# Optimization experiments

Measured on AMD Instinct MI355X. Metric: run time of the kernel, lower is better.

## Reference

```python
import jax, jax.numpy as jnp
import numpy as np

B, L, DIM, DQK = 4, 8192, 512, 512
THRESH = 0.5
TARGET_N = 6.0
RATIO_W = 0.03
LR_DIFF = 0.75
EPS = 1e-8


def setup_inputs() -> dict:
    key = jax.random.key(0)
    k1, k2, k3 = jax.random.split(key, 3)
    tokens = jax.random.normal(k1, (B, L, DIM), dtype=jnp.float32)
    # Linear(dim, 2*dqk, bias=False) weight, torch layout [out, in]
    Wqk = jax.random.normal(k2, (2 * DQK, DIM), dtype=jnp.float32) / np.sqrt(DIM).astype(np.float32)
    start_key = jax.random.normal(k3, (DQK,), dtype=jnp.float32) * 0.01  # heads=1
    return {"tokens": tokens, "Wqk": Wqk, "start_key": start_key}


def _straight_through(t, value):
    return t + jax.lax.stop_gradient(value - t)


def _frac_gradient(t, frac):
    # forward = t, backward grad scaled by frac
    return _straight_through(t * frac, t)


def _cosine_sim(a, b):
    dot = jnp.sum(a * b, axis=-1)
    na = jnp.maximum(jnp.sqrt(jnp.sum(a * a, axis=-1)), EPS)
    nb = jnp.maximum(jnp.sqrt(jnp.sum(b * b, axis=-1)), EPS)
    return dot / (na * nb)


def _assoc_scan(gates, x):
    # h_t = gates_t * h_{t-1} + x_t along axis 1 (inclusive first-order scan)
    def comb(l, r):
        al, bl = l
        ar, br = r
        return al * ar, br + ar * bl
    _, h = jax.lax.associative_scan(comb, (gates[..., None], x), axis=1)
    return h


def reference(tokens, Wqk, start_key):
    Bn, Ln, D = tokens.shape
    qk = jnp.einsum('bnd,ed->bne', tokens, Wqk)          # [B, L, 2*DQK]
    queries, keys = qk[..., :DQK], qk[..., DQK:]
    # key for position i is key_{i-1}, with learned start key at position 0
    keys_shift = jnp.concatenate(
        [jnp.broadcast_to(start_key, (Bn, 1, DQK)), keys[:, :-1]], axis=1)
    cos = _cosine_sim(queries, keys_shift)               # [B, L]
    probs = (1.0 - cos) * 0.5
    boundary = (probs > THRESH).at[:, 0].set(True)       # [B, L] bool
    num_chunks = boundary.sum(axis=-1)                   # [B]

    # stable compaction: boundary positions first, in order
    order = jnp.argsort(jnp.logical_not(boundary).astype(jnp.int32), axis=1)  # [B, L]
    ar = jnp.arange(Ln)
    chunk_mask = ar[None, :] < num_chunks[:, None]       # valid chunk slots
    pos = jnp.where(chunk_mask, order, Ln)               # boundary positions, sentinel L
    next_pos = jnp.concatenate([pos[:, 1:], jnp.full((Bn, 1), Ln, dtype=pos.dtype)], axis=1)
    chunk_lens = jnp.where(chunk_mask, next_pos - pos, 0)  # [B, L] int

    gathered = jnp.take_along_axis(tokens, order[..., None], axis=1)  # [B, L, D]
    boundary_probs = jnp.where(chunk_mask, jnp.take_along_axis(probs, order, axis=1), 0.0)
    gates = 1.0 - boundary_probs                         # padded slots -> 1 (matches torch, never read)
    downsampled = gathered * boundary_probs[..., None]   # padded slots -> 0

    confidence = jnp.where(boundary, probs, 1.0 - probs)
    scale = _straight_through(confidence, 1.0)           # forward value 1.0

    # aux ratio loss (with straight-through soft boundary fraction)
    Nt = TARGET_N
    F_hard = boundary.astype(probs.dtype)
    F_soft = jax.nn.sigmoid(probs - THRESH)
    F = _straight_through(F_soft, F_hard)
    Gm = probs.mean(axis=-1)
    Fm = F.mean(axis=-1)
    aux = (Nt / (Nt - 1.0)) * ((Nt - 1.0) * Fm * Gm + (1.0 - Fm) * (1.0 - Gm))
    weighted_aux_loss = aux.mean() * RATIO_W

    downsampled_out = _frac_gradient(downsampled, 1.0 / LR_DIFF)

    # ---- upsample path (the returned closure in the torch module) ----
    scanned = _assoc_scan(gates, downsampled_out)        # smooth across chunks
    rank = jnp.cumsum(boundary.astype(jnp.int32), axis=1) - 1  # chunk id of each token
    upsampled = jnp.take_along_axis(scanned, rank[..., None], axis=1)  # [B, L, D]
    upsampled = upsampled * scale[..., None]
    upsampled = _frac_gradient(upsampled, LR_DIFF)

    return downsampled_out, upsampled, weighted_aux_loss
```

## Files before the change

kernel.cpp:

```cpp
#include <hip/hip_runtime.h>
#include <cstdint>
#include <cstddef>

#define L 8192
#define BATCH 4
#define DQK 512
#define M_TOT (BATCH*L)
#define NSEG 128
#define SEGC 64
#define EPSC 1e-8f

typedef __attribute__((ext_vector_type(8))) short bf16x8;
typedef __attribute__((ext_vector_type(4))) float f32x4;
typedef __attribute__((ext_vector_type(8))) unsigned short u16x8;

__device__ __forceinline__ unsigned short bf16_rne(float x) {
  union { float f; unsigned u; } v; v.f = x;
  unsigned r = v.u + 0x7fffu + ((v.u >> 16) & 1u);
  return (unsigned short)(r >> 16);
}
__device__ __forceinline__ float bf16_tof(unsigned short b) {
  union { unsigned u; float f; } v; v.u = ((unsigned)b) << 16;
  return v.f;
}
__device__ __forceinline__ void gload_lds16(const void* g, void* l) {
  __builtin_amdgcn_global_load_lds(
      (const __attribute__((address_space(1))) unsigned int*)g,
      (__attribute__((address_space(3))) unsigned int*)l, 16, 0, 0);
}

__global__ __launch_bounds__(256) void k_split(const float* __restrict__ tokens,
                                               const float* __restrict__ Wqk,
                                               unsigned short* __restrict__ A1,
                                               unsigned short* __restrict__ A2,
                                               unsigned short* __restrict__ A3,
                                               unsigned short* __restrict__ W1,
                                               unsigned short* __restrict__ W2,
                                               unsigned short* __restrict__ W3) {
  const float* src; unsigned short *d1, *d2, *d3; size_t e0;
  if (blockIdx.x < 8192) {
    src = tokens; d1 = A1; d2 = A2; d3 = A3;
    e0 = ((size_t)blockIdx.x * 256 + threadIdx.x) * 8;
  } else {
    src = Wqk; d1 = W1; d2 = W2; d3 = W3;
    e0 = ((size_t)(blockIdx.x - 8192) * 256 + threadIdx.x) * 8;
  }
  float v[8];
  *(float4*)&v[0] = *(const float4*)(src + e0);
  *(float4*)&v[4] = *(const float4*)(src + e0 + 4);
  unsigned short o1[8], o2[8], o3[8];
  #pragma unroll
  for (int j = 0; j < 8; ++j) {
    float x = v[j];
    unsigned short b1 = bf16_rne(x);
    float r1 = x - bf16_tof(b1);
    unsigned short b2 = bf16_rne(r1);
    float r2 = r1 - bf16_tof(b2);
    unsigned short b3 = bf16_rne(r2);
    o1[j] = b1; o2[j] = b2; o3[j] = b3;
  }
  *(u16x8*)(d1 + e0) = *(u16x8*)o1;
  *(u16x8*)(d2 + e0) = *(u16x8*)o2;
  *(u16x8*)(d3 + e0) = *(u16x8*)o3;
}

__global__ __launch_bounds__(256, 3) void k_gemm_bf16(
    const unsigned short* __restrict__ A1, const unsigned short* __restrict__ A2,
    const unsigned short* __restrict__ A3,
    const unsigned short* __restrict__ W1, const unsigned short* __restrict__ W2,
    const unsigned short* __restrict__ W3,
    float* __restrict__ C) {
  __shared__ unsigned short lds[6 * 512 * 8];
  const int g = (blockIdx.x & 7) * 256 + (blockIdx.x >> 3);
  const int bx = g & 7;
  const int by = g >> 3;
  const int t = threadIdx.x;
  const int lane = t & 63;
  const int w = t >> 6;
  const int wr = w >> 1, wc = w & 1;

  f32x4 acc[4][4];
  #pragma unroll
  for (int i = 0; i < 4; ++i)
    #pragma unroll
    for (int j = 0; j < 4; ++j) acc[i][j] = (f32x4){0.f, 0.f, 0.f, 0.f};

  const unsigned short* srcA[3] = {A1, A2, A3};
  const unsigned short* srcW[3] = {W1, W2, W3};
  const int arow = by * 128;
  const int wrow = bx * 128;
  const int kg = lane >> 4;
  const int fr = lane & 15;

  for (int ks = 0; ks < 16; ++ks) {
    __syncthreads();
    const int kofs = ks * 32;
    #pragma unroll
    for (int s = 0; s < 3; ++s) {
      #pragma unroll
      for (int it = 0; it < 2; ++it) {
        const int p = it * 256 + t;
        const int row = p & 127, pg = p >> 7;
        gload_lds16(srcA[s] + (size_t)(arow + row) * 512 + kofs + pg * 8,
                    &lds[(s * 512 + p) * 8]);
        gload_lds16(srcW[s] + (size_t)(wrow + row) * 512 + kofs + pg * 8,
                    &lds[((3 + s) * 512 + p) * 8]);
      }
    }
    __syncthreads();

    bf16x8 bfr[4][3];
    #pragma unroll
    for (int nf = 0; nf < 4; ++nf) {
      const int row = wc * 64 + nf * 16 + fr;
      #pragma unroll
      for (int s = 0; s < 3; ++s)
        bfr[nf][s] = *(const bf16x8*)&lds[(((3 + s) * 512) + kg * 128 + row) * 8];
    }
    #pragma unroll
    for (int mf = 0; mf < 4; ++mf) {
      const int row = wr * 64 + mf * 16 + fr;
      bf16x8 a1 = *(const bf16x8*)&lds[((0 * 512) + kg * 128 + row) * 8];
      bf16x8 a2 = *(const bf16x8*)&lds[((1 * 512) + kg * 128 + row) * 8];
      bf16x8 a3 = *(const bf16x8*)&lds[((2 * 512) + kg * 128 + row) * 8];
      #pragma unroll
      for (int nf = 0; nf < 4; ++nf) {
        f32x4 c = acc[mf][nf];
        c = __builtin_amdgcn_mfma_f32_16x16x32_bf16(a1, bfr[nf][0], c, 0, 0, 0);
        c = __builtin_amdgcn_mfma_f32_16x16x32_bf16(a1, bfr[nf][1], c, 0, 0, 0);
        c = __builtin_amdgcn_mfma_f32_16x16x32_bf16(a2, bfr[nf][0], c, 0, 0, 0);
        c = __builtin_amdgcn_mfma_f32_16x16x32_bf16(a2, bfr[nf][1], c, 0, 0, 0);
        c = __builtin_amdgcn_mfma_f32_16x16x32_bf16(a1, bfr[nf][2], c, 0, 0, 0);
        c = __builtin_amdgcn_mfma_f32_16x16x32_bf16(a3, bfr[nf][0], c, 0, 0, 0);
        acc[mf][nf] = c;
      }
    }
  }
  const int fq = lane >> 4;
  #pragma unroll
  for (int mf = 0; mf < 4; ++mf) {
    #pragma unroll
    for (int nf = 0; nf < 4; ++nf) {
      const int col = bx * 128 + wc * 64 + nf * 16 + fr;
      #pragma unroll
      for (int r = 0; r < 4; ++r) {
        const int rrow = by * 128 + wr * 64 + mf * 16 + fq * 4 + r;
        C[(size_t)rrow * 1024 + col] = acc[mf][nf][r];
      }
    }
  }
}

__global__ __launch_bounds__(256) void k_gemm(const float* __restrict__ A,
                                              const float* __restrict__ W,
                                              float* __restrict__ C) {
  __shared__ float As[8][128];
  __shared__ float Bs[8][128];
  const int bx = blockIdx.x & 7;
  const int by = blockIdx.x >> 3;
  const int t  = threadIdx.x;
  const int tx = t & 15, ty = t >> 4;
  const int lr = t >> 1;
  const int lc = (t & 1) * 4;
  const float* Ag = A + (size_t)(by*128 + lr)*512 + lc;
  const float* Wg = W + (size_t)(bx*128 + lr)*512 + lc;
  float acc[8][8];
  #pragma unroll
  for (int i=0;i<8;i++)
    #pragma unroll
    for (int j=0;j<8;j++) acc[i][j]=0.f;

  for (int k0 = 0; k0 < 512; k0 += 8) {
    float4 av = *(const float4*)(Ag + k0);
    float4 bv = *(const float4*)(Wg + k0);
    __syncthreads();
    As[lc+0][lr]=av.x; As[lc+1][lr]=av.y; As[lc+2][lr]=av.z; As[lc+3][lr]=av.w;
    Bs[lc+0][lr]=bv.x; Bs[lc+1][lr]=bv.y; Bs[lc+2][lr]=bv.z; Bs[lc+3][lr]=bv.w;
    __syncthreads();
    #pragma unroll
    for (int kk=0;kk<8;kk++) {
      float af[8], bf[8];
      *(float4*)&af[0] = *(const float4*)&As[kk][ty*8];
      *(float4*)&af[4] = *(const float4*)&As[kk][ty*8+4];
      *(float4*)&bf[0] = *(const float4*)&Bs[kk][tx*8];
      *(float4*)&bf[4] = *(const float4*)&Bs[kk][tx*8+4];
      #pragma unroll
      for (int i=0;i<8;i++)
        #pragma unroll
        for (int j=0;j<8;j++)
          acc[i][j] = fmaf(af[i], bf[j], acc[i][j]);
    }
  }
  const int crow = by*128 + ty*8;
  const int ccol = bx*128 + tx*8;
  #pragma unroll
  for (int i=0;i<8;i++) {
    float* cp = C + (size_t)(crow+i)*1024 + ccol;
    *(float4*)cp     = make_float4(acc[i][0],acc[i][1],acc[i][2],acc[i][3]);
    *(float4*)(cp+4) = make_float4(acc[i][4],acc[i][5],acc[i][6],acc[i][7]);
  }
}

__global__ __launch_bounds__(256) void k_cos(const float* __restrict__ qk,
                                             const float* __restrict__ start_key,
                                             float* __restrict__ probs) {
  const int wid = threadIdx.x >> 6;
  const int lane = threadIdx.x & 63;
  const int p = blockIdx.x*4 + wid;
  const int n = p & (L-1);
  const float* q  = qk + (size_t)p*1024;
  const float* ks = (n==0) ? start_key : (qk + (size_t)(p-1)*1024 + 512);
  float dot=0.f, nq=0.f, nk=0.f;
  const int e0 = lane*8;
  #pragma unroll
  for (int j=0;j<8;j+=4) {
    float4 qv = *(const float4*)(q+e0+j);
    float4 kv = *(const float4*)(ks+e0+j);
    dot = fmaf(qv.x,kv.x,dot); dot = fmaf(qv.y,kv.y,dot);
    dot = fmaf(qv.z,kv.z,dot); dot = fmaf(qv.w,kv.w,dot);
    nq  = fmaf(qv.x,qv.x,nq);  nq  = fmaf(qv.y,qv.y,nq);
    nq  = fmaf(qv.z,qv.z,nq);  nq  = fmaf(qv.w,qv.w,nq);
    nk  = fmaf(kv.x,kv.x,nk);  nk  = fmaf(kv.y,kv.y,nk);
    nk  = fmaf(kv.z,kv.z,nk);  nk  = fmaf(kv.w,kv.w,nk);
  }
  #pragma unroll
  for (int m=32;m>=1;m>>=1) {
    dot += __shfl_xor(dot,m);
    nq  += __shfl_xor(nq,m);
    nk  += __shfl_xor(nk,m);
  }
  if (lane==0) {
    float na = fmaxf(sqrtf(nq), EPSC);
    float nb = fmaxf(sqrtf(nk), EPSC);
    float c  = dot/(na*nb);
    probs[p] = 0.5f*(1.f - c);
  }
}

__global__ __launch_bounds__(1024) void k_scan_bd(const float* __restrict__ probs,
                                                  int* __restrict__ bpos,
                                                  int* __restrict__ num_chunks,
                                                  float* __restrict__ auxvals) {
  const int b = blockIdx.x;
  const float* pb = probs + b*L;
  const int t = threadIdx.x;
  float pv[8]; int bd[8];
  const int base = t*8;
  float psum=0.f; int cnt=0;
  #pragma unroll
  for (int j=0;j<8;j++) {
    pv[j] = pb[base+j];
    bd[j] = (base+j == 0) || (pv[j] > 0.5f);
    cnt += bd[j];
    psum += pv[j];
  }
  const int lane = t & 63, w = t >> 6;
  int x = cnt;
  #pragma unroll
  for (int off=1; off<64; off<<=1) {
    int y = __shfl_up(x, off);
    if (lane >= off) x += y;
  }
  float ps = psum;
  #pragma unroll
  for (int m=32;m>=1;m>>=1) ps += __shfl_xor(ps, m);
  __shared__ int wsum[16]; __shared__ int wpre[17]; __shared__ float fsum[16];
  if (lane == 63) wsum[w] = x;
  if (lane == 0)  fsum[w] = ps;
  __syncthreads();
  if (t == 0) {
    int run = 0; float tot = 0.f;
    for (int i=0;i<16;i++) { wpre[i] = run; run += wsum[i]; tot += fsum[i]; }
    wpre[16] = run;
    num_chunks[b] = run;
    float Gm = tot / (float)L;
    float Fm = (float)run / (float)L;
    auxvals[b] = 1.2f * (5.f*Fm*Gm + (1.f-Fm)*(1.f-Gm));
  }
  __syncthreads();
  int rank = wpre[w] + (x - cnt);
  #pragma unroll
  for (int j=0;j<8;j++) {
    if (bd[j]) { bpos[b*L + rank] = base + j; rank++; }
  }
}

__global__ __launch_bounds__(512) void k_scan_local(const float* __restrict__ tokens,
                                                    const float* __restrict__ probs,
                                                    const int* __restrict__ bpos,
                                                    const int* __restrict__ num_chunks,
                                                    float* __restrict__ hend,
                                                    float* __restrict__ Pseg,
                                                    float* __restrict__ down) {
  const int b = blockIdx.x / NSEG;
  const int s = blockIdx.x - b * NSEG;
  const int c = threadIdx.x;
  const int nc = num_chunks[b];
  const int i0 = s*SEGC;
  const int seg = b*NSEG + s;
  const int z0 = (i0 > nc) ? i0 : nc;
  for (int i = z0; i < i0 + SEGC; ++i)
    down[((size_t)(b*L + i))*512 + c] = 0.f;
  if (i0 >= nc) {
    hend[(size_t)seg*512 + c] = 0.f;
    if (c==0) Pseg[seg] = 1.f;
    return;
  }
  const int iend = (i0+SEGC < nc) ? i0+SEGC : nc;
  const int cntc = iend - i0;
  __shared__ float p_s[SEGC];
  __shared__ int n_s[SEGC];
  if (c < cntc) {
    int n = bpos[b*L + i0 + c];
    n_s[c] = n;
    p_s[c] = probs[b*L + n];
  }
  __syncthreads();
  float h = 0.f, gp = 1.f;
  for (int i = i0; i < iend; ++i) {
    const int ii = i - i0;
    const float p = p_s[ii];
    const float g = 1.f - p;
    const float x = tokens[((size_t)(b*L + n_s[ii]))*512 + c] * p;
    h = fmaf(g, h, x);
    gp *= g;
    down[((size_t)(b*L + i))*512 + c] = x;
  }
  hend[(size_t)seg*512 + c] = h;
  if (c==0) Pseg[seg] = gp;
}

__global__ __launch_bounds__(512) void k_seg_scan(const float* __restrict__ hend,
                                                  const float* __restrict__ Pseg,
                                                  float* __restrict__ carry_in) {
  const int b   = blockIdx.x >> 7;
  const int gch = blockIdx.x & 127;
  const int sg  = threadIdx.x & 127;
  const int cl  = threadIdx.x >> 7;
  const int ch  = gch*4 + cl;
  const int seg = b*NSEG + sg;
  float h = hend[(size_t)seg*512 + ch];
  float P = Pseg[seg];
  __shared__ float sh[512], sP[512];
  const int idx = cl*128 + sg;
  #pragma unroll
  for (int off=1; off<NSEG; off<<=1) {
    sh[idx] = h; sP[idx] = P;
    __syncthreads();
    if (sg >= off) {
      h = fmaf(P, sh[idx-off], h);
      P = P * sP[idx-off];
    }
    __syncthreads();
  }
  sh[idx] = h;
  __syncthreads();
  carry_in[(size_t)seg*512 + ch] = (sg==0) ? 0.f : sh[idx-1];
}

__global__ __launch_bounds__(512) void k_expand(const float* __restrict__ down,
                                                const float* __restrict__ probs,
                                                const int* __restrict__ bpos,
                                                const int* __restrict__ num_chunks,
                                                const float* __restrict__ carry_in,
                                                float* __restrict__ up) {
  const int b = blockIdx.x / NSEG;
  const int s = blockIdx.x - b * NSEG;
  const int c = threadIdx.x;
  const int nc = num_chunks[b];
  const int i0 = s*SEGC;
  if (i0 >= nc) return;
  const int iend = (i0+SEGC < nc) ? i0+SEGC : nc;
  const int cntc = iend - i0;
  __shared__ float p_s[SEGC];
  __shared__ int n_s[SEGC+1];
  if (c < cntc) {
    int n = bpos[b*L + i0 + c];
    n_s[c] = n;
    p_s[c] = probs[b*L + n];
  }
  if (c == 0)   n_s[cntc] = (iend < nc) ? bpos[b*L + iend] : L;
  __syncthreads();
  float h = carry_in[((size_t)(b*NSEG + s))*512 + c];
  for (int i = i0; i < iend; ++i) {
    const int ii = i - i0;
    const float g = 1.f - p_s[ii];
    const float x = down[((size_t)(b*L + i))*512 + c];
    h = fmaf(g, h, x);
    const int n0 = n_s[ii], n1 = n_s[ii+1];
    for (int n = n0; n < n1; ++n)
      up[((size_t)(b*L + n))*512 + c] = h;
  }
}

__global__ void k_final(const float* __restrict__ auxvals, float* __restrict__ outp) {
  outp[0] = (auxvals[0]+auxvals[1]+auxvals[2]+auxvals[3]) * 0.25f * 0.03f;
}

extern "C" void kernel_launch(void* const* d_in, const int* in_sizes, int n_in,
                              void* d_out, int out_size, void* d_ws, size_t ws_size,
                              hipStream_t stream) {
  const float* tokens    = (const float*)d_in[0];
  const float* Wqk       = (const float*)d_in[1];
  const float* start_key = (const float*)d_in[2];
  float* out  = (float*)d_out;
  float* down = out;
  float* up   = out + (size_t)M_TOT*512;
  float* qk   = out;

  char* ws = (char*)d_ws;
  const size_t A_BYTES = (size_t)M_TOT*512*2;
  const size_t W_BYTES = (size_t)1024*512*2;
  const size_t STAGED_BASE = 3*A_BYTES + 3*W_BYTES;
  const size_t SMALL_BYTES = (size_t)M_TOT*4*2 + (size_t)BATCH*NSEG*512*4*2
                           + (size_t)BATCH*NSEG*4 + BATCH*4*2 + 256;
  const bool staged = ws_size >= STAGED_BASE + SMALL_BYTES;

  unsigned short* A1 = (unsigned short*)ws;
  unsigned short* A2 = (unsigned short*)(ws + A_BYTES);
  unsigned short* A3 = (unsigned short*)(ws + 2*A_BYTES);
  unsigned short* W1 = (unsigned short*)(ws + 3*A_BYTES);
  unsigned short* W2 = (unsigned short*)(ws + 3*A_BYTES + W_BYTES);
  unsigned short* W3 = (unsigned short*)(ws + 3*A_BYTES + 2*W_BYTES);

  size_t off = staged ? STAGED_BASE : 0;
  float* probs    = (float*)(ws + off); off += (size_t)M_TOT*4;
  int*   bpos     = (int*)  (ws + off); off += (size_t)M_TOT*4;
  float* hend     = (float*)(ws + off); off += (size_t)BATCH*NSEG*512*4;
  float* carry_in = (float*)(ws + off); off += (size_t)BATCH*NSEG*512*4;
  float* Pseg     = (float*)(ws + off); off += (size_t)BATCH*NSEG*4;
  int*   num_chunks = (int*)(ws + off); off += (size_t)BATCH*4;
  float* auxvals  = (float*)(ws + off); off += (size_t)BATCH*4;

  if (staged) {
    k_split<<<8448, 256, 0, stream>>>(tokens, Wqk, A1, A2, A3, W1, W2, W3);
    k_gemm_bf16<<<2048, 256, 0, stream>>>(A1, A2, A3, W1, W2, W3, qk);
  } else {
    k_gemm<<<2048, 256, 0, stream>>>(tokens, Wqk, qk);
  }
  k_cos<<<M_TOT/4, 256, 0, stream>>>(qk, start_key, probs);
  k_scan_bd<<<BATCH, 1024, 0, stream>>>(probs, bpos, num_chunks, auxvals);
  k_scan_local<<<BATCH*NSEG, 512, 0, stream>>>(tokens, probs, bpos, num_chunks,
                                               hend, Pseg, down);
  k_seg_scan<<<BATCH*NSEG, 512, 0, stream>>>(hend, Pseg, carry_in);
  k_expand<<<BATCH*NSEG, 512, 0, stream>>>(down, probs, bpos, num_chunks, carry_in, up);
  k_final<<<1, 1, 0, stream>>>(auxvals, out + (size_t)2*M_TOT*512);
}
```

Before: 368.6 us.

## Fuse cosine-similarity reductions into GEMM epilogue, avoiding qk materialization

Result: slower. 586.3 us (+59.1%).

```diff
diff --git a/kernel.cpp b/kernel.cpp
--- a/kernel.cpp
+++ b/kernel.cpp
@@ -64,20 +64,29 @@
   *(u16x8*)(d3 + e0) = *(u16x8*)o3;
 }
 
-__global__ __launch_bounds__(256, 3) void k_gemm_bf16(
+__global__ __launch_bounds__(256) void k_zero3(float* __restrict__ buf) {
+  buf[blockIdx.x * 256 + threadIdx.x] = 0.f;
+}
+
+__global__ __launch_bounds__(512, 4) void k_gemm_fused(
     const unsigned short* __restrict__ A1, const unsigned short* __restrict__ A2,
     const unsigned short* __restrict__ A3,
     const unsigned short* __restrict__ W1, const unsigned short* __restrict__ W2,
     const unsigned short* __restrict__ W3,
-    float* __restrict__ C) {
-  __shared__ unsigned short lds[6 * 512 * 8];
-  const int g = (blockIdx.x & 7) * 256 + (blockIdx.x >> 3);
-  const int bx = g & 7;
-  const int by = g >> 3;
+    float* __restrict__ dotv, float* __restrict__ nqrow, float* __restrict__ nkrow,
+    float* __restrict__ qstr, float* __restrict__ kstr) {
+  __shared__ unsigned short lds[9 * 512 * 8];
+  const int g = (blockIdx.x & 7) * 128 + (blockIdx.x >> 3);
+  const int cg = g & 3;
+  const int by = g >> 2;
   const int t = threadIdx.x;
   const int lane = t & 63;
   const int w = t >> 6;
-  const int wr = w >> 1, wc = w & 1;
+  const int wr = w >> 2;
+  const int wq = w & 3;
+  const int kg = lane >> 4;
+  const int fr = lane & 15;
+  const int fq = lane >> 4;
 
   f32x4 acc[4][4];
   #pragma unroll
@@ -88,34 +97,31 @@
   const unsigned short* srcA[3] = {A1, A2, A3};
   const unsigned short* srcW[3] = {W1, W2, W3};
   const int arow = by * 128;
-  const int wrow = bx * 128;
-  const int kg = lane >> 4;
-  const int fr = lane & 15;
-
+  const int btile = 3 + ((wq >= 2) ? 3 : 0);
+  const int colbase = (wq & 1) * 64;
+
+  const int ldrow = t & 127, ldkg = t >> 7;
   for (int ks = 0; ks < 16; ++ks) {
     __syncthreads();
-    const int kofs = ks * 32;
+    const int kofs = ks * 32 + ldkg * 8;
     #pragma unroll
     for (int s = 0; s < 3; ++s) {
-      #pragma unroll
-      for (int it = 0; it < 2; ++it) {
-        const int p = it * 256 + t;
-        const int row = p & 127, pg = p >> 7;
-        gload_lds16(srcA[s] + (size_t)(arow + row) * 512 + kofs + pg * 8,
-                    &lds[(s * 512 + p) * 8]);
-        gload_lds16(srcW[s] + (size_t)(wrow + row) * 512 + kofs + pg * 8,
-                    &lds[((3 + s) * 512 + p) * 8]);
-      }
+      gload_lds16(srcA[s] + (size_t)(arow + ldrow) * 512 + kofs,
+                  &lds[((s) * 512 + t) * 8]);
+      gload_lds16(srcW[s] + (size_t)(cg * 128 + ldrow) * 512 + kofs,
+                  &lds[((3 + s) * 512 + t) * 8]);
+      gload_lds16(srcW[s] + (size_t)(512 + cg * 128 + ldrow) * 512 + kofs,
+                  &lds[((6 + s) * 512 + t) * 8]);
     }
     __syncthreads();
 
     bf16x8 bfr[4][3];
     #pragma unroll
     for (int nf = 0; nf < 4; ++nf) {
-      const int row = wc * 64 + nf * 16 + fr;
+      const int row = colbase + nf * 16 + fr;
       #pragma unroll
       for (int s = 0; s < 3; ++s)
-        bfr[nf][s] = *(const bf16x8*)&lds[(((3 + s) * 512) + kg * 128 + row) * 8];
+        bfr[nf][s] = *(const bf16x8*)&lds[(((btile + s) * 512) + kg * 128 + row) * 8];
     }
     #pragma unroll
     for (int mf = 0; mf < 4; ++mf) {
@@ -136,19 +142,117 @@
       }
     }
   }
-  const int fq = lane >> 4;
-  #pragma unroll
-  for (int mf = 0; mf < 4; ++mf) {
-    #pragma unroll
-    for (int nf = 0; nf < 4; ++nf) {
-      const int col = bx * 128 + wc * 64 + nf * 16 + fr;
+
+  float* kbuf = (float*)lds;
+  __syncthreads();
+  if (wq >= 2) {
+    #pragma unroll
+    for (int mf = 0; mf < 4; ++mf)
+      #pragma unroll
+      for (int nf = 0; nf < 4; ++nf)
+        #pragma unroll
+        for (int r = 0; r < 4; ++r)
+          kbuf[(wr*64 + mf*16 + fq*4 + r) * 132 + colbase + nf*16 + fr] = acc[mf][nf][r];
+  }
+  __syncthreads();
+
+  if (wq < 2) {
+    #pragma unroll
+    for (int mf = 0; mf < 4; ++mf) {
       #pragma unroll
       for (int r = 0; r < 4; ++r) {
-        const int rrow = by * 128 + wr * 64 + mf * 16 + fq * 4 + r;
-        C[(size_t)rrow * 1024 + col] = acc[mf][nf][r];
+        const int row = wr*64 + mf*16 + fq*4 + r;
+        float v = 0.f, nqv = 0.f;
+        #pragma unroll
+        for (int nf = 0; nf < 4; ++nf) {
+          const float qv = acc[mf][nf][r];
+          nqv = fmaf(qv, qv, nqv);
+          if (row > 0)
+            v = fmaf(qv, kbuf[(row-1)*132 + colbase + nf*16 + fr], v);
+        }
+        #pragma unroll
+        for (int m = 1; m < 16; m <<= 1) {
+          v   += __shfl_xor(v, m);
+          nqv += __shfl_xor(nqv, m);
+        }
+        if (fr == 0) {
+          const int gp = by*128 + row;
+          atomicAdd(&nqrow[gp], nqv);
+          if (row > 0) atomicAdd(&dotv[gp], v);
+        }
       }
     }
-  }
+    if (wr == 0 && fq == 0) {
+      #pragma unroll
+      for (int nf = 0; nf < 4; ++nf)
+        qstr[(size_t)by*512 + cg*128 + colbase + nf*16 + fr] = acc[0][nf][0];
+    }
+  } else {
+    #pragma unroll
+    for (int mf = 0; mf < 4; ++mf) {
+      #pragma unroll
+      for (int r = 0; r < 4; ++r) {
+        const int row = wr*64 + mf*16 + fq*4 + r;
+        float nkv = 0.f;
+        #pragma unroll
+        for (int nf = 0; nf < 4; ++nf) {
+          const float kv = acc[mf][nf][r];
+          nkv = fmaf(kv, kv, nkv);
+        }
+        #pragma unroll
+        for (int m = 1; m < 16; m <<= 1) nkv += __shfl_xor(nkv, m);
+        if (fr == 0) atomicAdd(&nkrow[by*128 + row], nkv);
+      }
+    }
+    if (wr == 1 && fq == 3) {
+      #pragma unroll
+      for (int nf = 0; nf < 4; ++nf)
+        kstr[(size_t)by*512 + cg*128 + colbase + nf*16 + fr] = acc[3][nf][3];
+    }
+  }
+}
+
+__global__ __launch_bounds__(256) void k_straddle(const float* __restrict__ qstr,
+                                                  const float* __restrict__ kstr,
+                                                  const float* __restrict__ skey,
+                                                  const float* __restrict__ nkrow,
+                                                  float* __restrict__ dotv,
+                                                  float* __restrict__ nkS) {
+  const int tile = blockIdx.x * 4 + (threadIdx.x >> 6);
+  const int lane = threadIdx.x & 63;
+  const int p = tile * 128;
+  const bool isStart = ((tile & 63) == 0);
+  const float* q  = qstr + (size_t)tile * 512;
+  const float* pk = isStart ? skey : (kstr + (size_t)(tile - 1) * 512);
+  float v = 0.f, u = 0.f;
+  const int e0 = lane * 8;
+  #pragma unroll
+  for (int j = 0; j < 8; j += 4) {
+    float4 qv = *(const float4*)(q + e0 + j);
+    float4 kv = *(const float4*)(pk + e0 + j);
+    v = fmaf(qv.x,kv.x,v); v = fmaf(qv.y,kv.y,v);
+    v = fmaf(qv.z,kv.z,v); v = fmaf(qv.w,kv.w,v);
+    u = fmaf(kv.x,kv.x,u); u = fmaf(kv.y,kv.y,u);
+    u = fmaf(kv.z,kv.z,u); u = fmaf(kv.w,kv.w,u);
+  }
+  #pragma unroll
+  for (int m = 32; m >= 1; m >>= 1) { v += __shfl_xor(v,m); u += __shfl_xor(u,m); }
+  if (lane == 0) {
+    dotv[p] = v;
+    nkS[tile] = isStart ? u : nkrow[p - 1];
+  }
+}
+
+__global__ __launch_bounds__(256) void k_probs(const float* __restrict__ dotv,
+                                               const float* __restrict__ nqrow,
+                                               const float* __restrict__ nkrow,
+                                               const float* __restrict__ nkS,
+                                               float* __restrict__ probs) {
+  const int i = blockIdx.x * 256 + threadIdx.x;
+  const float nq = nqrow[i];
+  const float nk = ((i & 127) == 0) ? nkS[i >> 7] : nkrow[i - 1];
+  const float c = dotv[i] / (fmaxf(sqrtf(nq), EPSC) * fmaxf(sqrtf(nk), EPSC));
+  probs[i] = 0.5f * (1.f - c);
 }
 
 __global__ __launch_bounds__(256) void k_gemm(const float* __restrict__ A,
@@ -332,7 +436,11 @@
 
 __global__ __launch_bounds__(512) void k_seg_scan(const float* __restrict__ hend,
                                                   const float* __restrict__ Pseg,
-                                                  float* __restrict__ carry_in) {
+                                                  float* __restrict__ carry_in,
+                                                  const float* __restrict__ auxvals,
+                                                  float* __restrict__ outp) {
+  if (blockIdx.x == 0 && threadIdx.x == 0)
+    outp[0] = (auxvals[0]+auxvals[1]+auxvals[2]+auxvals[3]) * 0.25f * 0.03f;
   const int b   = blockIdx.x >> 7;
   const int gch = blockIdx.x & 127;
   const int sg  = threadIdx.x & 127;
@@ -393,10 +501,6 @@
   }
 }
 
-__global__ void k_final(const float* __restrict__ auxvals, float* __restrict__ outp) {
-  outp[0] = (auxvals[0]+auxvals[1]+auxvals[2]+auxvals[3]) * 0.25f * 0.03f;
-}
-
 extern "C" void kernel_launch(void* const* d_in, const int* in_sizes, int n_in,
                               void* d_out, int out_size, void* d_ws, size_t ws_size,
                               hipStream_t stream) {
@@ -413,7 +517,8 @@
   const size_t W_BYTES = (size_t)1024*512*2;
   const size_t STAGED_BASE = 3*A_BYTES + 3*W_BYTES;
   const size_t SMALL_BYTES = (size_t)M_TOT*4*2 + (size_t)BATCH*NSEG*512*4*2
-                           + (size_t)BATCH*NSEG*4 + BATCH*4*2 + 256;
+                           + (size_t)BATCH*NSEG*4 + BATCH*4*2
+                           + (size_t)M_TOT*4*3 + 256*4 + (size_t)256*512*4*2 + 1024;
   const bool staged = ws_size >= STAGED_BASE + SMALL_BYTES;
 
   unsigned short* A1 = (unsigned short*)ws;
@@ -431,18 +536,28 @@
   float* Pseg     = (float*)(ws + off); off += (size_t)BATCH*NSEG*4;
   int*   num_chunks = (int*)(ws + off); off += (size_t)BATCH*4;
   float* auxvals  = (float*)(ws + off); off += (size_t)BATCH*4;
+  float* dotv     = (float*)(ws + off); off += (size_t)M_TOT*4;
+  float* nqrow    = (float*)(ws + off); off += (size_t)M_TOT*4;
+  float* nkrow    = (float*)(ws + off); off += (size_t)M_TOT*4;
+  float* nkS      = (float*)(ws + off); off += 256*4;
+  float* qstr     = (float*)(ws + off); off += (size_t)256*512*4;
+  float* kstr     = (float*)(ws + off); off += (size_t)256*512*4;
 
   if (staged) {
     k_split<<<8448, 256, 0, stream>>>(tokens, Wqk, A1, A2, A3, W1, W2, W3);
-    k_gemm_bf16<<<2048, 256, 0, stream>>>(A1, A2, A3, W1, W2, W3, qk);
+    k_zero3<<<(3*M_TOT)/256, 256, 0, stream>>>(dotv);
+    k_gemm_fused<<<1024, 512, 0, stream>>>(A1, A2, A3, W1, W2, W3,
+                                           dotv, nqrow, nkrow, qstr, kstr);
+    k_straddle<<<64, 256, 0, stream>>>(qstr, kstr, start_key, nkrow, dotv, nkS);
+    k_probs<<<M_TOT/256, 256, 0, stream>>>(dotv, nqrow, nkrow, nkS, probs);
   } else {
     k_gemm<<<2048, 256, 0, stream>>>(tokens, Wqk, qk);
-  }
-  k_cos<<<M_TOT/4, 256, 0, stream>>>(qk, start_key, probs);
+    k_cos<<<M_TOT/4, 256, 0, stream>>>(qk, start_key, probs);
+  }
   k_scan_bd<<<BATCH, 1024, 0, stream>>>(probs, bpos, num_chunks, auxvals);
   k_scan_local<<<BATCH*NSEG, 512, 0, stream>>>(tokens, probs, bpos, num_chunks,
                                                hend, Pseg, down);
-  k_seg_scan<<<BATCH*NSEG, 512, 0, stream>>>(hend, Pseg, carry_in);
+  k_seg_scan<<<BATCH*NSEG, 512, 0, stream>>>(hend, Pseg, carry_in,
+                                             auxvals, out + (size_t)2*M_TOT*512);
   k_expand<<<BATCH*NSEG, 512, 0, stream>>>(down, probs, bpos, num_chunks, carry_in, up);
-  k_final<<<1, 1, 0, stream>>>(auxvals, out + (size_t)2*M_TOT*512);
-}
+}
```
